# Performance work log

Measured on AMD Instinct MI355X. Metric: run time of the kernel, lower is better.

Reference implementation:

```python
import jax, jax.numpy as jnp
import numpy as np

D = 768; NH = 12; HD = D // NH; L = 12; NC = 27; PATCH = 16; MLP = 3072; PROJ = 512
IMG = 224; GRID = IMG // PATCH; HW = GRID * GRID; S = NC + HW
NEG = -1e9

def _ln(x, w, b):
    m = jnp.mean(x, -1, keepdims=True)
    v = jnp.mean(jnp.square(x - m), -1, keepdims=True)
    return (x - m) * jax.lax.rsqrt(v + 1e-5) * w + b

def _quick_gelu(x):
    return x * jax.nn.sigmoid(1.702 * x)

def _build_mask(attn_obj_masks, dtype):
    # CRIS block mask: cls<->cls blocked except self; cls->patch allowed only for
    # patches of that class; patch->cls blocked; patch->patch fully allowed.
    B = attn_obj_masks.shape[0]
    oh = jax.nn.one_hot(attn_obj_masks, NC, dtype=dtype)              # [B, HW, NC]
    T11 = jnp.broadcast_to(1.0 - jnp.eye(NC, dtype=dtype), (B, NC, NC))
    M13 = 1.0 - jnp.swapaxes(oh, 1, 2)                                # [B, NC, HW]
    top = jnp.concatenate([T11, M13], axis=2)
    bot = jnp.concatenate([jnp.ones((B, HW, NC), dtype), jnp.zeros((B, HW, HW), dtype)], axis=2)
    Mb = jnp.concatenate([top, bot], axis=1)                          # [B, S, S]
    return jnp.where(Mb == 1.0, jnp.asarray(NEG, dtype), jnp.asarray(0.0, dtype))

def reference(img, sents, attn_obj_masks, obj_masks, cls_tokens, patch_w, patch_b, pos_embed,
              ln1_w, ln1_b, qkv_w, qkv_b, out_w, out_b, ln2_w, ln2_b,
              mlp_w1, mlp_b1, mlp_w2, mlp_b2, ln_post_w, ln_post_b, proj):
    B = img.shape[0]
    sents = sents / jnp.linalg.norm(sents, axis=-1, keepdims=True)    # encode_text output, L2 normed
    mask = _build_mask(attn_obj_masks, img.dtype)                     # [B, S, S]
    # patch embedding (conv stride 16) -> [B, HW, D]
    p = jax.lax.conv_general_dilated(img, patch_w, (PATCH, PATCH), 'VALID',
                                     dimension_numbers=('NCHW', 'OIHW', 'NCHW'))
    p = p.reshape(B, D, HW).transpose(0, 2, 1) + patch_b
    x = jnp.concatenate([jnp.broadcast_to(cls_tokens, (B, NC, D)), p], axis=1) + pos_embed
    scale = 1.0 / np.sqrt(HD).astype(np.float32)
    def block(x, prm):
        l1w, l1b, qw, qb, ow, ob, l2w, l2b, w1, b1, w2, b2 = prm
        h = _ln(x, l1w, l1b)
        qkv = h @ qw + qb
        q, k, v = jnp.split(qkv, 3, axis=-1)
        q = q.reshape(B, S, NH, HD).transpose(0, 2, 1, 3)
        k = k.reshape(B, S, NH, HD).transpose(0, 2, 1, 3)
        v = v.reshape(B, S, NH, HD).transpose(0, 2, 1, 3)
        scores = jnp.einsum('bhqd,bhkd->bhqk', q, k) * scale + mask[:, None]
        a = jax.nn.softmax(scores, axis=-1)
        o = jnp.einsum('bhqk,bhkd->bhqd', a, v).transpose(0, 2, 1, 3).reshape(B, S, D)
        x = x + o @ ow + ob
        h = _ln(x, l2w, l2b)
        x = x + _quick_gelu(h @ w1 + b1) @ w2 + b2
        return x, None
    x, _ = jax.lax.scan(block, x, (ln1_w, ln1_b, qkv_w, qkv_b, out_w, out_b,
                                   ln2_w, ln2_b, mlp_w1, mlp_b1, mlp_w2, mlp_b2))
    tokens = _ln(x, ln_post_w, ln_post_b) @ proj                      # [B, S, PROJ]
    obj = tokens[:, :NC]
    obj = obj / jnp.linalg.norm(obj, axis=-1, keepdims=True)
    pred_id = jnp.einsum('bnd,bd->bn', obj, sents)                    # [B, NC]
    # per-class scatter loop == gather of pred_id by per-pixel class id
    pred = jnp.take_along_axis(pred_id, obj_masks.reshape(B, -1), axis=1).reshape(obj_masks.shape)
    return pred                                                       # [B, 224, 224]

def setup_inputs():
    B = 16; std = 0.02
    ks = jax.random.split(jax.random.key(0), 16)
    f = jax.random.normal
    return {
        'img': f(ks[0], (B, 3, IMG, IMG), jnp.float32),
        'sents': f(ks[1], (B, PROJ), jnp.float32),
        'attn_obj_masks': jax.random.randint(ks[2], (B, HW), 0, NC, jnp.int32),
        'obj_masks': jax.random.randint(ks[3], (B, IMG, IMG), 0, NC, jnp.int32),
        'cls_tokens': f(ks[4], (1, NC, D)) * std,
        'patch_w': f(ks[5], (D, 3, PATCH, PATCH)) * std,
        'patch_b': jnp.zeros((D,)),
        'pos_embed': f(ks[6], (S, D)) * std,
        'ln1_w': jnp.ones((L, D)), 'ln1_b': jnp.zeros((L, D)),
        'qkv_w': f(ks[7], (L, D, 3 * D)) * std, 'qkv_b': jnp.zeros((L, 3 * D)),
        'out_w': f(ks[8], (L, D, D)) * std, 'out_b': jnp.zeros((L, D)),
        'ln2_w': jnp.ones((L, D)), 'ln2_b': jnp.zeros((L, D)),
        'mlp_w1': f(ks[9], (L, D, MLP)) * std, 'mlp_b1': jnp.zeros((L, MLP)),
        'mlp_w2': f(ks[10], (L, MLP, D)) * std, 'mlp_b2': jnp.zeros((L, D)),
        'ln_post_w': jnp.ones((D,)), 'ln_post_b': jnp.zeros((D,)),
        'proj': f(ks[11], (D, PROJ)) * std,
    }
```

## Files before the change

kernel.cpp:

```cpp
#include <hip/hip_runtime.h>

#define DEV __device__ __forceinline__

typedef short bf16x8 __attribute__((ext_vector_type(8)));
typedef float f32x4 __attribute__((ext_vector_type(4)));
typedef int vi4 __attribute__((ext_vector_type(4)));
typedef unsigned short u16;

#define NEGV -1000000000.0f

DEV u16 f2bf(float f) {
  union { float f; unsigned u; } v; v.f = f;
  unsigned r = v.u + 0x7FFFu + ((v.u >> 16) & 1u);
  return (u16)(r >> 16);
}

DEV bf16x8 ld_bf8(const u16* p) {
  vi4 v = *(const vi4*)p;
  return __builtin_bit_cast(bf16x8, v);
}

DEV void gload_lds16(const u16* g, vi4* l) {
  __builtin_amdgcn_global_load_lds((const __attribute__((address_space(1))) void*)g,
                                   (__attribute__((address_space(3))) void*)l, 16, 0, 0);
}

template<int BN, int MODE, bool GELU, int KS>
__global__ __launch_bounds__(256) void gemm_bt(
    const u16* __restrict__ A, const u16* __restrict__ Bt,
    const float* __restrict__ bias,
    float* __restrict__ Cf, u16* __restrict__ Cb,
    int M, int N, int K, const float* __restrict__ pos)
{
  constexpr int FJ = BN / 32;
  constexpr int LB = BN / 64;
  constexpr int LTOT = 2 + LB;
  __shared__ vi4 As[2][512];
  __shared__ vi4 Bs[2][BN * 4];

  int gx = gridDim.x, gy = gridDim.y;
  int nwg = gx * gy * (int)gridDim.z;
  int orig = blockIdx.x + gx * (blockIdx.y + gy * blockIdx.z);
  int qq = nwg >> 3, rr = nwg & 7;
  int xcd = orig & 7, off = orig >> 3;
  int id = (xcd < rr) ? xcd * (qq + 1) + off : rr * (qq + 1) + (xcd - rr) * qq + off;
  int bx = id % gx, rest = id / gx, by = rest % gy, bz = rest / gy;

  int tid = threadIdx.x, lane = tid & 63, wid = tid >> 6;
  int wm = wid >> 1, wn = wid & 1;
  int m0 = by * 128, n0 = bx * BN;
  int kBeg = (K / KS) * bz, kEnd = kBeg + K / KS;
  f32x4 acc[4][FJ] = {};

  auto STAGE = [&](int buf, int kk) {
    #pragma unroll
    for (int r = 0; r < 2; ++r) {
      int flat = r * 256 + tid;
      int row = flat >> 2, c = flat & 3;
      int cs = c ^ ((row >> 1) & 3);
      gload_lds16(A + (long)(m0 + row) * K + kk + cs * 8, &As[buf][r * 256 + wid * 64]);
    }
    #pragma unroll
    for (int r = 0; r < LB; ++r) {
      int flat = r * 256 + tid;
      int row = flat >> 2, c = flat & 3;
      int cs = c ^ ((row >> 1) & 3);
      gload_lds16(Bt + (long)(n0 + row) * K + kk + cs * 8, &Bs[buf][r * 256 + wid * 64]);
    }
  };

  STAGE(0, kBeg);
  int cur = 0;
  for (int kk = kBeg; kk < kEnd; kk += 32) {
    if (kk + 32 < kEnd) {
      STAGE(cur ^ 1, kk + 32);
      asm volatile("s_waitcnt vmcnt(%0)" :: "i"(LTOT) : "memory");
    } else {
      asm volatile("s_waitcnt vmcnt(0)" ::: "memory");
    }
    __builtin_amdgcn_s_barrier();
    bf16x8 af[4], bfr[FJ];
    int cg = lane >> 4, l15 = lane & 15;
    #pragma unroll
    for (int i = 0; i < 4; ++i) {
      int ra = wm * 64 + i * 16 + l15;
      af[i] = __builtin_bit_cast(bf16x8, As[cur][ra * 4 + (cg ^ ((ra >> 1) & 3))]);
    }
    #pragma unroll
    for (int j = 0; j < FJ; ++j) {
      int rb = wn * (BN / 2) + j * 16 + l15;
      bfr[j] = __builtin_bit_cast(bf16x8, Bs[cur][rb * 4 + (cg ^ ((rb >> 1) & 3))]);
    }
    #pragma unroll
    for (int i = 0; i < 4; ++i)
      #pragma unroll
      for (int j = 0; j < FJ; ++j)
        acc[i][j] = __builtin_amdgcn_mfma_f32_16x16x32_bf16(af[i], bfr[j], acc[i][j], 0, 0, 0);
    __builtin_amdgcn_s_barrier();
    cur ^= 1;
  }

  int cg = lane >> 4, l15 = lane & 15;
  #pragma unroll
  for (int i = 0; i < 4; ++i) {
    #pragma unroll
    for (int j = 0; j < FJ; ++j) {
      int col = n0 + wn * (BN / 2) + j * 16 + l15;
      float bv = bias ? bias[col] : 0.f;
      #pragma unroll
      for (int r = 0; r < 4; ++r) {
        int row = m0 + wm * 64 + i * 16 + cg * 4 + r;
        if (row < M) {
          float v = acc[i][j][r];
          if (KS == 1 || bz == 0) v += bv;
          if (GELU) v = v / (1.f + __expf(-1.702f * v));
          if (MODE == 0) Cb[(long)row * N + col] = f2bf(v);
          else if (MODE == 1) {
            if (KS > 1) atomicAdd(&Cf[(long)row * N + col], v);
            else Cf[(long)row * N + col] += v;
          }
          else if (MODE == 2) Cf[(long)row * N + col] = v;
          else {
            int hw = row % 196;
            int xr = (row / 196) * 223 + 27 + hw;
            Cf[(long)xr * 768 + col] = v + pos[(27 + hw) * 768 + col];
          }
        }
      }
    }
  }
}

__global__ __launch_bounds__(256) void attn_kernel(
    const u16* __restrict__ QKV, const int* __restrict__ aom, u16* __restrict__ O)
{
  __shared__ vi4 Kl[224 * 8];
  __shared__ vi4 Vt[64 * 28];
  __shared__ vi4 Pl[4][16 * 28];
  __shared__ int ml[196];
  int tid = threadIdx.x, lane = tid & 63, wid = tid >> 6;
  int qg = blockIdx.x, h = blockIdx.y, b = blockIdx.z;
  long rowbase = (long)b * 223;
  #pragma unroll
  for (int it = 0; it < 7; ++it) {
    int flat = it * 256 + tid;
    int s = flat >> 3, c = flat & 7;
    vi4 v = {0, 0, 0, 0};
    if (s < 223) v = *(const vi4*)(QKV + (rowbase + s) * 2304 + 768 + h * 64 + c * 8);
    Kl[s * 8 + (c ^ (s & 7))] = v;
  }
  u16* vt16 = (u16*)Vt;
  #pragma unroll
  for (int it = 0; it < 7; ++it) {
    int flat = it * 256 + tid;
    int s = flat >> 3, c = flat & 7;
    vi4 v = {0, 0, 0, 0};
    if (s < 223) v = *(const vi4*)(QKV + (rowbase + s) * 2304 + 1536 + h * 64 + c * 8);
    union { vi4 v4; u16 hx[8]; } uu; uu.v4 = v;
    int cs = s >> 3;
    #pragma unroll
    for (int j = 0; j < 8; ++j) {
      int d = c * 8 + j;
      vt16[d * 224 + (cs ^ ((d >> 1) & 3)) * 8 + (s & 7)] = uu.hx[j];
    }
  }
  for (int i = tid; i < 196; i += 256) ml[i] = aom[b * 196 + i];
  __syncthreads();

  int qf = qg * 4 + wid;
  if (qf >= 14) return;
  int q0 = qf * 16;
  int colk = lane & 15, cg = lane >> 4;
  int arow = q0 + colk; if (arow > 222) arow = 222;
  const u16* qb = QKV + (rowbase + arow) * 2304 + h * 64;
  bf16x8 aq0 = ld_bf8(qb + cg * 8);
  bf16x8 aq1 = ld_bf8(qb + 32 + cg * 8);

  f32x4 sc[14];
  #pragma unroll
  for (int kf = 0; kf < 14; ++kf) {
    int key = kf * 16 + colk;
    f32x4 a = {0.f, 0.f, 0.f, 0.f};
    bf16x8 bk0 = __builtin_bit_cast(bf16x8, Kl[key * 8 + (cg ^ (key & 7))]);
    bf16x8 bk1 = __builtin_bit_cast(bf16x8, Kl[key * 8 + ((4 + cg) ^ (key & 7))]);
    a = __builtin_amdgcn_mfma_f32_16x16x32_bf16(aq0, bk0, a, 0, 0, 0);
    a = __builtin_amdgcn_mfma_f32_16x16x32_bf16(aq1, bk1, a, 0, 0, 0);
    sc[kf] = a;
  }
  #pragma unroll
  for (int r = 0; r < 4; ++r) {
    int q = q0 + cg * 4 + r;
    float mx = -3.4e38f;
    #pragma unroll
    for (int kf = 0; kf < 14; ++kf) {
      int key = kf * 16 + colk;
      float mval;
      if (key >= 223) mval = NEGV;
      else if (q >= 27) mval = (key < 27) ? NEGV : 0.f;
      else if (key < 27) mval = (key == q) ? 0.f : NEGV;
      else mval = (ml[key - 27] == q) ? 0.f : NEGV;
      float s = sc[kf][r] * 0.125f + mval;
      sc[kf][r] = s;
      mx = fmaxf(mx, s);
    }
    #pragma unroll
    for (int d = 1; d < 16; d <<= 1) mx = fmaxf(mx, __shfl_xor(mx, d));
    float sum = 0.f;
    #pragma unroll
    for (int kf = 0; kf < 14; ++kf) {
      float e = __expf(sc[kf][r] - mx);
      sc[kf][r] = e; sum += e;
    }
    #pragma unroll
    for (int d = 1; d < 16; d <<= 1) sum += __shfl_xor(sum, d);
    float inv = 1.f / sum;
    #pragma unroll
    for (int kf = 0; kf < 14; ++kf) sc[kf][r] *= inv;
  }
  u16* pw = (u16*)Pl[wid];
  #pragma unroll
  for (int kf = 0; kf < 14; ++kf) {
    int key = kf * 16 + colk;
    int ck = key >> 3;
    #pragma unroll
    for (int r = 0; r < 4; ++r) {
      int prow = cg * 4 + r;
      pw[prow * 224 + (ck ^ ((prow >> 1) & 3)) * 8 + (key & 7)] = f2bf(sc[kf][r]);
    }
  }
  f32x4 oacc[4] = {};
  #pragma unroll
  for (int ks = 0; ks < 7; ++ks) {
    bf16x8 pa = __builtin_bit_cast(bf16x8, Pl[wid][colk * 28 + ((ks * 4 + cg) ^ ((colk >> 1) & 3))]);
    #pragma unroll
    for (int nf = 0; nf < 4; ++nf) {
      int d = nf * 16 + colk;
      bf16x8 bv = __builtin_bit_cast(bf16x8, Vt[d * 28 + ((ks * 4 + cg) ^ ((d >> 1) & 3))]);
      oacc[nf] = __builtin_amdgcn_mfma_f32_16x16x32_bf16(pa, bv, oacc[nf], 0, 0, 0);
    }
  }
  #pragma unroll
  for (int nf = 0; nf < 4; ++nf) {
    int d = h * 64 + nf * 16 + colk;
    #pragma unroll
    for (int r = 0; r < 4; ++r) {
      int q = q0 + cg * 4 + r;
      if (q < 223) O[(rowbase + q) * 768 + d] = f2bf(oacc[nf][r]);
    }
  }
}

template<bool MAP27>
__global__ __launch_bounds__(256) void ln_kernel(
    const float* __restrict__ X, u16* __restrict__ Hb,
    const float* __restrict__ w, const float* __restrict__ bb)
{
  __shared__ float sb[8];
  int r = blockIdx.x;
  int xr = MAP27 ? (r / 27) * 223 + (r % 27) : r;
  const float* xp = X + (long)xr * 768;
  int t = threadIdx.x;
  float v0 = xp[t], v1 = xp[t + 256], v2 = xp[t + 512];
  float s = v0 + v1 + v2;
  #pragma unroll
  for (int d = 1; d < 64; d <<= 1) s += __shfl_xor(s, d);
  if ((t & 63) == 0) sb[t >> 6] = s;
  __syncthreads();
  float mean = (sb[0] + sb[1] + sb[2] + sb[3]) * (1.f / 768.f);
  float d0 = v0 - mean, d1 = v1 - mean, d2 = v2 - mean;
  float q = d0 * d0 + d1 * d1 + d2 * d2;
  #pragma unroll
  for (int d = 1; d < 64; d <<= 1) q += __shfl_xor(q, d);
  if ((t & 63) == 0) sb[4 + (t >> 6)] = q;
  __syncthreads();
  float var = (sb[4] + sb[5] + sb[6] + sb[7]) * (1.f / 768.f);
  float rs = rsqrtf(var + 1e-5f);
  Hb[(long)r * 768 + t]       = f2bf(d0 * rs * w[t] + bb[t]);
  Hb[(long)r * 768 + t + 256] = f2bf(d1 * rs * w[t + 256] + bb[t + 256]);
  Hb[(long)r * 768 + t + 512] = f2bf(d2 * rs * w[t + 512] + bb[t + 512]);
}

__global__ __launch_bounds__(256) void transpose_w(
    const float* __restrict__ W, u16* __restrict__ WT, int K, int N, long sW, long sT)
{
  __shared__ float t[64][65];
  int z = blockIdx.z;
  W += (long)z * sW; WT += (long)z * sT;
  int n0 = blockIdx.x * 64, k0 = blockIdx.y * 64;
  #pragma unroll
  for (int i = 0; i < 16; ++i) {
    int flat = i * 256 + threadIdx.x;
    int r = flat >> 6, c = flat & 63;
    t[r][c] = W[(long)(k0 + r) * N + n0 + c];
  }
  __syncthreads();
  #pragma unroll
  for (int i = 0; i < 16; ++i) {
    int flat = i * 256 + threadIdx.x;
    int rn = flat >> 6, ck = flat & 63;
    WT[(long)(n0 + rn) * K + k0 + ck] = f2bf(t[ck][rn]);
  }
}

__global__ void convert_bf16(const float* __restrict__ src, u16* __restrict__ dst, int n) {
  int i = blockIdx.x * 256 + threadIdx.x;
  if (i < n) dst[i] = f2bf(src[i]);
}

__global__ __launch_bounds__(256) void patch_extract(const float* __restrict__ img, u16* __restrict__ Xp) {
  int row = blockIdx.x;
  int b = row / 196, hw = row % 196, gh = hw / 14, gw = hw % 14;
  for (int idx = threadIdx.x; idx < 768; idx += 256) {
    int cch = idx >> 8, rem = idx & 255, kh = rem >> 4, kw = rem & 15;
    Xp[(long)row * 768 + idx] = f2bf(img[((long)(b * 3 + cch) * 224 + gh * 16 + kh) * 224 + gw * 16 + kw]);
  }
}

__global__ void cls_pos_fill(const float* __restrict__ cls, const float* __restrict__ pos, float* __restrict__ x) {
  int i = blockIdx.x * 256 + threadIdx.x;
  if (i >= 16 * 27 * 768) return;
  int d = i % 768, t = i / 768, b = t / 27, s = t % 27;
  x[((long)b * 223 + s) * 768 + d] = cls[s * 768 + d] + pos[s * 768 + d];
}

__global__ __launch_bounds__(256) void sents_norm(const float* __restrict__ s, float* __restrict__ sn) {
  __shared__ float sb[4];
  int b = blockIdx.x, t = threadIdx.x;
  float v0 = s[b * 512 + t], v1 = s[b * 512 + t + 256];
  float q = v0 * v0 + v1 * v1;
  #pragma unroll
  for (int d = 1; d < 64; d <<= 1) q += __shfl_xor(q, d);
  if ((t & 63) == 0) sb[t >> 6] = q;
  __syncthreads();
  float inv = rsqrtf(sb[0] + sb[1] + sb[2] + sb[3]);
  sn[b * 512 + t] = v0 * inv;
  sn[b * 512 + t + 256] = v1 * inv;
}

__global__ __launch_bounds__(256) void obj_dot(const float* __restrict__ obj, const float* __restrict__ sn, float* __restrict__ pid) {
  __shared__ float sb[8];
  int r = blockIdx.x, t = threadIdx.x, b = r / 27;
  float v0 = obj[(long)r * 512 + t], v1 = obj[(long)r * 512 + t + 256];
  float w0 = sn[b * 512 + t], w1 = sn[b * 512 + t + 256];
  float q = v0 * v0 + v1 * v1;
  float dt = v0 * w0 + v1 * w1;
  #pragma unroll
  for (int d = 1; d < 64; d <<= 1) { q += __shfl_xor(q, d); dt += __shfl_xor(dt, d); }
  if ((t & 63) == 0) { sb[t >> 6] = q; sb[4 + (t >> 6)] = dt; }
  __syncthreads();
  if (t == 0) pid[r] = (sb[4] + sb[5] + sb[6] + sb[7]) * rsqrtf(sb[0] + sb[1] + sb[2] + sb[3]);
}

__global__ void gather_pred(const int* __restrict__ om, const float* __restrict__ pid, float* __restrict__ out) {
  int i = blockIdx.x * 256 + threadIdx.x;
  if (i >= 16 * 224 * 224) return;
  int b = i / (224 * 224);
  out[i] = pid[b * 27 + om[i]];
}

extern "C" void kernel_launch(void* const* d_in, const int* in_sizes, int n_in,
                              void* d_out, int out_size, void* d_ws, size_t ws_size,
                              hipStream_t stream) {
  const float* img     = (const float*)d_in[0];
  const float* sents   = (const float*)d_in[1];
  const int*   aom     = (const int*)d_in[2];
  const int*   omask   = (const int*)d_in[3];
  const float* cls     = (const float*)d_in[4];
  const float* patch_w = (const float*)d_in[5];
  const float* patch_b = (const float*)d_in[6];
  const float* pos     = (const float*)d_in[7];
  const float* ln1w    = (const float*)d_in[8];
  const float* ln1b    = (const float*)d_in[9];
  const float* qkvw    = (const float*)d_in[10];
  const float* qkvb    = (const float*)d_in[11];
  const float* outw    = (const float*)d_in[12];
  const float* outb    = (const float*)d_in[13];
  const float* ln2w    = (const float*)d_in[14];
  const float* ln2b    = (const float*)d_in[15];
  const float* m1w     = (const float*)d_in[16];
  const float* m1b     = (const float*)d_in[17];
  const float* m2w     = (const float*)d_in[18];
  const float* m2b     = (const float*)d_in[19];
  const float* lnpw    = (const float*)d_in[20];
  const float* lnpb    = (const float*)d_in[21];
  const float* projw   = (const float*)d_in[22];

  char* p = (char*)d_ws;
  auto alloc = [&](size_t bytes) { char* r = p; p += (bytes + 255) & ~(size_t)255; return r; };
  float* x   = (float*)alloc(3568ul * 768 * 4);
  u16* H     = (u16*)alloc(3584ul * 768 * 2);
  u16* QKV   = (u16*)alloc(3584ul * 2304 * 2);
  u16* Obuf  = (u16*)alloc(3584ul * 768 * 2);
  u16* G     = (u16*)alloc(3584ul * 3072 * 2);
  u16* PWc   = (u16*)alloc(768ul * 768 * 2);
  u16* PrT   = (u16*)alloc(512ul * 768 * 2);
  float* obj = (float*)alloc(432ul * 512 * 4);
  float* sn  = (float*)alloc(16ul * 512 * 4);
  float* pid = (float*)alloc(432ul * 4);

  const size_t wlayer = (2304ul * 768 + 768ul * 768 + 3072ul * 768 + 768ul * 3072) * 2;
  size_t used = (size_t)(p - (char*)d_ws);
  int nw = (ws_size >= used + 12 * wlayer + 65536) ? 12 : 1;
  const long sQ = 2304l * 768, sO = 768l * 768, s1 = 768l * 3072, s2 = 3072l * 768;
  u16* WqT = (u16*)alloc((size_t)sQ * 2 * nw);
  u16* WoT = (u16*)alloc((size_t)sO * 2 * nw);
  u16* W1T = (u16*)alloc((size_t)s1 * 2 * nw);
  u16* W2T = (u16*)alloc((size_t)s2 * 2 * nw);

  convert_bf16<<<2304, 256, 0, stream>>>(patch_w, PWc, 768 * 768);
  transpose_w<<<dim3(8, 12, 1), 256, 0, stream>>>(projw, PrT, 768, 512, 0, 0);
  if (nw == 12) {
    transpose_w<<<dim3(36, 12, 12), 256, 0, stream>>>(qkvw, WqT, 768, 2304, sQ, sQ);
    transpose_w<<<dim3(12, 12, 12), 256, 0, stream>>>(outw, WoT, 768, 768, sO, sO);
    transpose_w<<<dim3(48, 12, 12), 256, 0, stream>>>(m1w, W1T, 768, 3072, s1, s1);
    transpose_w<<<dim3(12, 48, 12), 256, 0, stream>>>(m2w, W2T, 3072, 768, s2, s2);
  }
  patch_extract<<<3136, 256, 0, stream>>>(img, H);
  cls_pos_fill<<<1296, 256, 0, stream>>>(cls, pos, x);
  gemm_bt<64, 3, false, 1><<<dim3(12, 25), 256, 0, stream>>>(H, PWc, patch_b, x, nullptr, 3136, 768, 768, pos);

  for (int l = 0; l < 12; ++l) {
    u16 *wq, *wo, *w1, *w2;
    if (nw == 12) { wq = WqT + (long)l * sQ; wo = WoT + (long)l * sO; w1 = W1T + (long)l * s1; w2 = W2T + (long)l * s2; }
    else {
      wq = WqT; wo = WoT; w1 = W1T; w2 = W2T;
      transpose_w<<<dim3(36, 12, 1), 256, 0, stream>>>(qkvw + (long)l * sQ, wq, 768, 2304, 0, 0);
      transpose_w<<<dim3(12, 12, 1), 256, 0, stream>>>(outw + (long)l * sO, wo, 768, 768, 0, 0);
      transpose_w<<<dim3(48, 12, 1), 256, 0, stream>>>(m1w + (long)l * s1, w1, 768, 3072, 0, 0);
      transpose_w<<<dim3(12, 48, 1), 256, 0, stream>>>(m2w + (long)l * s2, w2, 3072, 768, 0, 0);
    }
    ln_kernel<false><<<3568, 256, 0, stream>>>(x, H, ln1w + l * 768, ln1b + l * 768);
    gemm_bt<128, 0, false, 1><<<dim3(18, 28), 256, 0, stream>>>(H, wq, qkvb + l * 2304, nullptr, QKV, 3568, 2304, 768, nullptr);
    attn_kernel<<<dim3(4, 12, 16), 256, 0, stream>>>(QKV, aom, Obuf);
    gemm_bt<64, 1, false, 2><<<dim3(12, 28, 2), 256, 0, stream>>>(Obuf, wo, outb + l * 768, x, nullptr, 3568, 768, 768, nullptr);
    ln_kernel<false><<<3568, 256, 0, stream>>>(x, H, ln2w + l * 768, ln2b + l * 768);
    gemm_bt<128, 0, true, 1><<<dim3(24, 28), 256, 0, stream>>>(H, w1, m1b + l * 3072, nullptr, G, 3568, 3072, 768, nullptr);
    gemm_bt<64, 1, false, 2><<<dim3(12, 28, 2), 256, 0, stream>>>(G, w2, m2b + l * 768, x, nullptr, 3568, 768, 3072, nullptr);
  }

  ln_kernel<true><<<432, 256, 0, stream>>>(x, H, lnpw, lnpb);
  gemm_bt<64, 2, false, 1><<<dim3(8, 4), 256, 0, stream>>>(H, PrT, nullptr, obj, nullptr, 432, 512, 768, nullptr);
  sents_norm<<<16, 256, 0, stream>>>(sents, sn);
  obj_dot<<<432, 256, 0, stream>>>(obj, sn, pid);
  gather_pred<<<3136, 256, 0, stream>>>(omask, pid, (float*)d_out);
}
```

Measured before the change: 2.438 ms.

## Triple-buffer GEMM loads, halve attention grid, vectorize weight transpose

Several changes at once. The GEMM moves from a 2-stage to a 3-stage LDS pipeline, prefetching two K tiles ahead to hide more global load latency, at the cost of more LDS per block and possibly lower occupancy. The attention kernel loads K straight into LDS with global_load_lds, and each wave now handles two query fragments, so the grid halves and the K/V staging is amortized over twice the queries. The weight transpose uses float4 reads and packed 32-bit bf16 writes to reduce memory transactions.

```diff
diff --git a/kernel.cpp b/kernel.cpp
--- a/kernel.cpp
+++ b/kernel.cpp
@@ -35,8 +35,8 @@
   constexpr int FJ = BN / 32;
   constexpr int LB = BN / 64;
   constexpr int LTOT = 2 + LB;
-  __shared__ vi4 As[2][512];
-  __shared__ vi4 Bs[2][BN * 4];
+  __shared__ vi4 As[3][512];
+  __shared__ vi4 Bs[3][BN * 4];
 
   int gx = gridDim.x, gy = gridDim.y;
   int nwg = gx * gy * (int)gridDim.z;
@@ -49,7 +49,8 @@
   int tid = threadIdx.x, lane = tid & 63, wid = tid >> 6;
   int wm = wid >> 1, wn = wid & 1;
   int m0 = by * 128, n0 = bx * BN;
-  int kBeg = (K / KS) * bz, kEnd = kBeg + K / KS;
+  int kBeg = (K / KS) * bz;
+  int nT = (K / KS) >> 5;
   f32x4 acc[4][FJ] = {};
 
   auto STAGE = [&](int buf, int kk) {
@@ -70,10 +71,14 @@
   };
 
   STAGE(0, kBeg);
+  STAGE(1, kBeg + 32);
   int cur = 0;
-  for (int kk = kBeg; kk < kEnd; kk += 32) {
-    if (kk + 32 < kEnd) {
-      STAGE(cur ^ 1, kk + 32);
+  for (int t = 0; t < nT; ++t) {
+    int kk = kBeg + t * 32;
+    if (t + 2 < nT) {
+      STAGE((t + 2) % 3, kk + 64);
+      asm volatile("s_waitcnt vmcnt(%0)" :: "i"(2 * LTOT) : "memory");
+    } else if (t + 1 < nT) {
       asm volatile("s_waitcnt vmcnt(%0)" :: "i"(LTOT) : "memory");
     } else {
       asm volatile("s_waitcnt vmcnt(0)" ::: "memory");
@@ -97,7 +102,7 @@
       for (int j = 0; j < FJ; ++j)
         acc[i][j] = __builtin_amdgcn_mfma_f32_16x16x32_bf16(af[i], bfr[j], acc[i][j], 0, 0, 0);
     __builtin_amdgcn_s_barrier();
-    cur ^= 1;
+    cur = (cur + 1) % 3;
   }
 
   int cg = lane >> 4, l15 = lane & 15;
@@ -145,9 +150,8 @@
   for (int it = 0; it < 7; ++it) {
     int flat = it * 256 + tid;
     int s = flat >> 3, c = flat & 7;
-    vi4 v = {0, 0, 0, 0};
-    if (s < 223) v = *(const vi4*)(QKV + (rowbase + s) * 2304 + 768 + h * 64 + c * 8);
-    Kl[s * 8 + (c ^ (s & 7))] = v;
+    int cs = c ^ (s & 7);
+    gload_lds16(QKV + (rowbase + s) * 2304 + 768 + h * 64 + cs * 8, &Kl[it * 256 + wid * 64]);
   }
   u16* vt16 = (u16*)Vt;
   #pragma unroll
@@ -167,85 +171,89 @@
   for (int i = tid; i < 196; i += 256) ml[i] = aom[b * 196 + i];
   __syncthreads();
 
-  int qf = qg * 4 + wid;
-  if (qf >= 14) return;
-  int q0 = qf * 16;
   int colk = lane & 15, cg = lane >> 4;
-  int arow = q0 + colk; if (arow > 222) arow = 222;
-  const u16* qb = QKV + (rowbase + arow) * 2304 + h * 64;
-  bf16x8 aq0 = ld_bf8(qb + cg * 8);
-  bf16x8 aq1 = ld_bf8(qb + 32 + cg * 8);
-
-  f32x4 sc[14];
-  #pragma unroll
-  for (int kf = 0; kf < 14; ++kf) {
-    int key = kf * 16 + colk;
-    f32x4 a = {0.f, 0.f, 0.f, 0.f};
-    bf16x8 bk0 = __builtin_bit_cast(bf16x8, Kl[key * 8 + (cg ^ (key & 7))]);
-    bf16x8 bk1 = __builtin_bit_cast(bf16x8, Kl[key * 8 + ((4 + cg) ^ (key & 7))]);
-    a = __builtin_amdgcn_mfma_f32_16x16x32_bf16(aq0, bk0, a, 0, 0, 0);
-    a = __builtin_amdgcn_mfma_f32_16x16x32_bf16(aq1, bk1, a, 0, 0, 0);
-    sc[kf] = a;
-  }
-  #pragma unroll
-  for (int r = 0; r < 4; ++r) {
-    int q = q0 + cg * 4 + r;
-    float mx = -3.4e38f;
+  #pragma unroll
+  for (int rep = 0; rep < 2; ++rep) {
+    int fo = wid * 2 + rep;
+    if (fo >= 7) break;
+    int qf = qg * 7 + fo;
+    int q0 = qf * 16;
+    int arow = q0 + colk; if (arow > 222) arow = 222;
+    const u16* qb = QKV + (rowbase + arow) * 2304 + h * 64;
+    bf16x8 aq0 = ld_bf8(qb + cg * 8);
+    bf16x8 aq1 = ld_bf8(qb + 32 + cg * 8);
+
+    f32x4 sc[14];
     #pragma unroll
     for (int kf = 0; kf < 14; ++kf) {
       int key = kf * 16 + colk;
-      float mval;
-      if (key >= 223) mval = NEGV;
-      else if (q >= 27) mval = (key < 27) ? NEGV : 0.f;
-      else if (key < 27) mval = (key == q) ? 0.f : NEGV;
-      else mval = (ml[key - 27] == q) ? 0.f : NEGV;
-      float s = sc[kf][r] * 0.125f + mval;
-      sc[kf][r] = s;
-      mx = fmaxf(mx, s);
-    }
-    #pragma unroll
-    for (int d = 1; d < 16; d <<= 1) mx = fmaxf(mx, __shfl_xor(mx, d));
-    float sum = 0.f;
-    #pragma unroll
-    for (int kf = 0; kf < 14; ++kf) {
-      float e = __expf(sc[kf][r] - mx);
-      sc[kf][r] = e; sum += e;
-    }
-    #pragma unroll
-    for (int d = 1; d < 16; d <<= 1) sum += __shfl_xor(sum, d);
-    float inv = 1.f / sum;
-    #pragma unroll
-    for (int kf = 0; kf < 14; ++kf) sc[kf][r] *= inv;
-  }
-  u16* pw = (u16*)Pl[wid];
-  #pragma unroll
-  for (int kf = 0; kf < 14; ++kf) {
-    int key = kf * 16 + colk;
-    int ck = key >> 3;
-    #pragma unroll
-    for (int r = 0; r < 4; ++r) {
-      int prow = cg * 4 + r;
-      pw[prow * 224 + (ck ^ ((prow >> 1) & 3)) * 8 + (key & 7)] = f2bf(sc[kf][r]);
-    }
-  }
-  f32x4 oacc[4] = {};
-  #pragma unroll
-  for (int ks = 0; ks < 7; ++ks) {
-    bf16x8 pa = __builtin_bit_cast(bf16x8, Pl[wid][colk * 28 + ((ks * 4 + cg) ^ ((colk >> 1) & 3))]);
-    #pragma unroll
-    for (int nf = 0; nf < 4; ++nf) {
-      int d = nf * 16 + colk;
-      bf16x8 bv = __builtin_bit_cast(bf16x8, Vt[d * 28 + ((ks * 4 + cg) ^ ((d >> 1) & 3))]);
-      oacc[nf] = __builtin_amdgcn_mfma_f32_16x16x32_bf16(pa, bv, oacc[nf], 0, 0, 0);
-    }
-  }
-  #pragma unroll
-  for (int nf = 0; nf < 4; ++nf) {
-    int d = h * 64 + nf * 16 + colk;
+      f32x4 a = {0.f, 0.f, 0.f, 0.f};
+      bf16x8 bk0 = __builtin_bit_cast(bf16x8, Kl[key * 8 + (cg ^ (key & 7))]);
+      bf16x8 bk1 = __builtin_bit_cast(bf16x8, Kl[key * 8 + ((4 + cg) ^ (key & 7))]);
+      a = __builtin_amdgcn_mfma_f32_16x16x32_bf16(aq0, bk0, a, 0, 0, 0);
+      a = __builtin_amdgcn_mfma_f32_16x16x32_bf16(aq1, bk1, a, 0, 0, 0);
+      sc[kf] = a;
+    }
     #pragma unroll
     for (int r = 0; r < 4; ++r) {
       int q = q0 + cg * 4 + r;
-      if (q < 223) O[(rowbase + q) * 768 + d] = f2bf(oacc[nf][r]);
+      float mx = -3.4e38f;
+      #pragma unroll
+      for (int kf = 0; kf < 14; ++kf) {
+        int key = kf * 16 + colk;
+        float mval;
+        if (key >= 223) mval = NEGV;
+        else if (q >= 27) mval = (key < 27) ? NEGV : 0.f;
+        else if (key < 27) mval = (key == q) ? 0.f : NEGV;
+        else mval = (ml[key - 27] == q) ? 0.f : NEGV;
+        float s = sc[kf][r] * 0.125f + mval;
+        sc[kf][r] = s;
+        mx = fmaxf(mx, s);
+      }
+      #pragma unroll
+      for (int d = 1; d < 16; d <<= 1) mx = fmaxf(mx, __shfl_xor(mx, d));
+      float sum = 0.f;
+      #pragma unroll
+      for (int kf = 0; kf < 14; ++kf) {
+        float e = __expf(sc[kf][r] - mx);
+        sc[kf][r] = e; sum += e;
+      }
+      #pragma unroll
+      for (int d = 1; d < 16; d <<= 1) sum += __shfl_xor(sum, d);
+      float inv = 1.f / sum;
+      #pragma unroll
+      for (int kf = 0; kf < 14; ++kf) sc[kf][r] *= inv;
+    }
+    u16* pw = (u16*)Pl[wid];
+    #pragma unroll
+    for (int kf = 0; kf < 14; ++kf) {
+      int key = kf * 16 + colk;
+      int ck = key >> 3;
+      #pragma unroll
+      for (int r = 0; r < 4; ++r) {
+        int prow = cg * 4 + r;
+        pw[prow * 224 + (ck ^ ((prow >> 1) & 3)) * 8 + (key & 7)] = f2bf(sc[kf][r]);
+      }
+    }
+    f32x4 oacc[4] = {};
+    #pragma unroll
+    for (int ks = 0; ks < 7; ++ks) {
+      bf16x8 pa = __builtin_bit_cast(bf16x8, Pl[wid][colk * 28 + ((ks * 4 + cg) ^ ((colk >> 1) & 3))]);
+      #pragma unroll
+      for (int nf = 0; nf < 4; ++nf) {
+        int d = nf * 16 + colk;
+        bf16x8 bv = __builtin_bit_cast(bf16x8, Vt[d * 28 + ((ks * 4 + cg) ^ ((d >> 1) & 3))]);
+        oacc[nf] = __builtin_amdgcn_mfma_f32_16x16x32_bf16(pa, bv, oacc[nf], 0, 0, 0);
+      }
+    }
+    #pragma unroll
+    for (int nf = 0; nf < 4; ++nf) {
+      int d = h * 64 + nf * 16 + colk;
+      #pragma unroll
+      for (int r = 0; r < 4; ++r) {
+        int q = q0 + cg * 4 + r;
+        if (q < 223) O[(rowbase + q) * 768 + d] = f2bf(oacc[nf][r]);
+      }
     }
   }
 }
@@ -288,17 +296,19 @@
   W += (long)z * sW; WT += (long)z * sT;
   int n0 = blockIdx.x * 64, k0 = blockIdx.y * 64;
   #pragma unroll
-  for (int i = 0; i < 16; ++i) {
+  for (int i = 0; i < 4; ++i) {
     int flat = i * 256 + threadIdx.x;
-    int r = flat >> 6, c = flat & 63;
-    t[r][c] = W[(long)(k0 + r) * N + n0 + c];
-  }
-  __syncthreads();
-  #pragma unroll
-  for (int i = 0; i < 16; ++i) {
+    int r = flat >> 4, c = (flat & 15) * 4;
+    float4 v = *(const float4*)(W + (long)(k0 + r) * N + n0 + c);
+    t[r][c] = v.x; t[r][c + 1] = v.y; t[r][c + 2] = v.z; t[r][c + 3] = v.w;
+  }
+  __syncthreads();
+  #pragma unroll
+  for (int i = 0; i < 8; ++i) {
     int flat = i * 256 + threadIdx.x;
-    int rn = flat >> 6, ck = flat & 63;
-    WT[(long)(n0 + rn) * K + k0 + ck] = f2bf(t[ck][rn]);
+    int rn = flat >> 5, ck = (flat & 31) * 2;
+    unsigned val = (unsigned)f2bf(t[ck][rn]) | ((unsigned)f2bf(t[ck + 1][rn]) << 16);
+    *(unsigned*)(WT + (long)(n0 + rn) * K + k0 + ck) = val;
   }
 }
 
@@ -431,7 +441,7 @@
     }
     ln_kernel<false><<<3568, 256, 0, stream>>>(x, H, ln1w + l * 768, ln1b + l * 768);
     gemm_bt<128, 0, false, 1><<<dim3(18, 28), 256, 0, stream>>>(H, wq, qkvb + l * 2304, nullptr, QKV, 3568, 2304, 768, nullptr);
-    attn_kernel<<<dim3(4, 12, 16), 256, 0, stream>>>(QKV, aom, Obuf);
+    attn_kernel<<<dim3(2, 12, 16), 256, 0, stream>>>(QKV, aom, Obuf);
     gemm_bt<64, 1, false, 2><<<dim3(12, 28, 2), 256, 0, stream>>>(Obuf, wo, outb + l * 768, x, nullptr, 3568, 768, 768, nullptr);
     ln_kernel<false><<<3568, 256, 0, stream>>>(x, H, ln2w + l * 768, ln2b + l * 768);
     gemm_bt<128, 0, true, 1><<<dim3(24, 28), 256, 0, stream>>>(H, w1, m1b + l * 3072, nullptr, G, 3568, 3072, 768, nullptr);
```

New measurement: 2.440 ms. No clear change (+0.1%).
